# Optimization experiments

Measured on AMD Instinct MI355X. Metric: run time of the kernel, lower is better.

Reference implementation:

```python
import jax, jax.numpy as jnp
import numpy as np

# ---- static config (from init_kwargs) ----
XB = (-51.2, 51.2, 0.8); YB = (-51.2, 51.2, 0.8); ZB = (-10.0, 10.0, 20.0); DB = (1.0, 60.0, 1.0)
OGH, OGW = 256, 704          # image_size
DS = 16                      # downsample
C_IN, C_TR = 512, 64         # numC_input, numC_trans
B, N = 2, 6                  # batch, cameras
FH, FW = (OGH + DS - 1) // DS, (OGW + DS - 1) // DS   # 16, 44
DBINS = int(np.arange(DB[0], DB[1], DB[2]).shape[0])  # 59 depth bins
NX = int(round((XB[1] - XB[0]) / XB[2]))              # 128
NY = int(round((YB[1] - YB[0]) / YB[2]))              # 128
NZ = int(round((ZB[1] - ZB[0]) / ZB[2]))              # 1
START = jnp.array([XB[0], YB[0], ZB[0]], jnp.float32)
INTERVAL = jnp.array([XB[2], YB[2], ZB[2]], jnp.float32)

def make_frustum():
    ds = np.arange(DB[0], DB[1], DB[2], dtype=np.float32)            # [D]
    xs = np.linspace(0.0, OGW - 1, FW, dtype=np.float32)             # [FW]
    ys = np.linspace(0.0, OGH - 1, FH, dtype=np.float32)             # [FH]
    x, y, d = np.broadcast_arrays(xs[None, None, :], ys[None, :, None], ds[:, None, None])
    return jnp.asarray(np.stack([x, y, d], -1))                      # [D,FH,FW,3]

FRUSTUM = make_frustum()


def setup_inputs() -> dict:
    key = jax.random.key(0)
    k1, k2, k3 = jax.random.split(key, 3)
    x = jax.random.normal(k1, (B, N, C_IN, FH, FW), jnp.float32)
    # camera->ego rotation: cam z -> ego x, cam x -> -ego y, cam y -> -ego z
    R = jnp.array([[0., 0., 1.], [-1., 0., 0.], [0., -1., 0.]], jnp.float32)
    rots = jnp.broadcast_to(R, (B, N, 3, 3))
    trans = 0.5 * jax.random.normal(k2, (B, N, 3), jnp.float32)
    K = jnp.array([[500., 0., OGW / 2.], [0., 500., OGH / 2.], [0., 0., 1.]], jnp.float32)
    intrins = jnp.broadcast_to(K, (B, N, 3, 3))
    fan = C_IN + DBINS + C_TR
    w_depth = jax.random.normal(k3, (DBINS + C_TR, C_IN), jnp.float32) * np.float32(np.sqrt(2.0 / fan))
    b_depth = jnp.zeros((DBINS + C_TR,), jnp.float32)
    return {"x": x, "rots": rots, "trans": trans, "intrins": intrins,
            "w_depth": w_depth, "b_depth": b_depth}


def reference(x, rots, trans, intrins, w_depth, b_depth):
    # ---- geometry: frustum pixel coords -> ego frame (get_geometry) ----
    pts = jnp.concatenate([FRUSTUM[..., :2] * FRUSTUM[..., 2:3], FRUSTUM[..., 2:3]], -1)  # [D,FH,FW,3]
    combine = rots @ jnp.linalg.inv(intrins)                                              # [B,N,3,3]
    geom = jnp.einsum('bnij,dhwj->bndhwi', combine, pts) + trans[:, :, None, None, None, :]
    # ---- depth-weighted feature volume (get_volume) ----
    xf = x.reshape(B * N, C_IN, FH, FW)
    feat = jnp.einsum('oc,bchw->bohw', w_depth, xf) + b_depth[None, :, None, None]        # 1x1 conv
    depth = jax.nn.softmax(feat[:, :DBINS], axis=1)                                       # [BN,D,H,W]
    ctx = feat[:, DBINS:DBINS + C_TR]                                                     # [BN,C,H,W]
    vol = depth[:, None] * ctx[:, :, None]                                                # [BN,C,D,H,W]
    vol = vol.reshape(B, N, C_TR, DBINS, FH, FW).transpose(0, 1, 3, 4, 5, 2)              # [B,N,D,H,W,C]
    # ---- voxel pooling: sort/cumsum trick == per-voxel segment-sum scatter ----
    g = jnp.trunc((geom - START) / INTERVAL).astype(jnp.int32).reshape(-1, 3)             # trunc == torch .long()
    P = g.shape[0]
    b_ix = jnp.repeat(jnp.arange(B, dtype=jnp.int32), P // B)
    kept = ((g[:, 0] >= 0) & (g[:, 0] < NX) & (g[:, 1] >= 0) & (g[:, 1] < NY)
            & (g[:, 2] >= 0) & (g[:, 2] < NZ))
    total = B * NZ * NX * NY
    flat = ((b_ix * NZ + g[:, 2]) * NX + g[:, 0]) * NY + g[:, 1]                          # bev[b,gz,gx,gy]
    flat = jnp.where(kept, flat, total)                                                   # invalid -> dummy slot
    feats = jnp.where(kept[:, None], vol.reshape(-1, C_TR), 0.0)
    bev = jnp.zeros((total + 1, C_TR), vol.dtype).at[flat].add(feats)[:total]
    bev = bev.reshape(B, NZ, NX, NY, C_TR).transpose(0, 4, 1, 2, 3)                       # [B,C,NZ,NX,NY]
    return bev.reshape(B, C_TR * NZ, NX, NY)
```

## Files before the change

### kernel.cpp

```cpp
#include <hip/hip_runtime.h>
#include <cstddef>
#include <cstdint>
#include <math.h>

#define C_IN   512
#define C_TR   64
#define DBINS  59
#define NO     123
#define NOP    128
#define FH     16
#define FW     44
#define NPIX   704
#define NCAM   6
#define NBATCH 2
#define NBN    12
#define NXG    128
#define NYG    128
#define NCH    4
#define KCH    (C_IN/NCH)

#define WS_CMB     0
#define WS_XS      128
#define WS_YS      176

#define WSP_PART   256
#define PART_SZ    (NCH*NBN*NPIX*NOP)
#define WSP_DEP    (WSP_PART + PART_SZ)
#define DEP_SZ     (NBN*NPIX*C_TR)
#define WSP_CTX    (WSP_DEP + DEP_SZ)
#define WSP_BEV    (WSP_CTX + DEP_SZ)
#define BEV_SZ     (NBATCH*NXG*NYG*C_TR)
#define WS_FAST_TOTALF (WSP_BEV + BEV_SZ)

#define WS_FEAT    256
#define WS_CTX     (WS_FEAT + NBN*NOP*NPIX)
#define WS_BEV     (WS_CTX + NBN*NPIX*C_TR)

__global__ __launch_bounds__(256) void zero_kernel(float4* __restrict__ p, int n4)
{
  int i = blockIdx.x * 256 + threadIdx.x;
  const int stride = gridDim.x * 256;
  for (; i < n4; i += stride) p[i] = make_float4(0.f, 0.f, 0.f, 0.f);
}

__global__ __launch_bounds__(64) void prep_kernel(
    const float* __restrict__ rots, const float* __restrict__ intrins,
    float* __restrict__ wsf)
{
#pragma clang fp contract(off)
  int t = threadIdx.x;
  if (t < NBN) {
    const float* K = intrins + t * 9;
    const float* R = rots + t * 9;
    float A[3][3] = {{K[0],K[1],K[2]},{K[3],K[4],K[5]},{K[6],K[7],K[8]}};
    int piv[3] = {0,1,2};
    for (int k = 0; k < 2; ++k) {
      int p = k; float mx = fabsf(A[k][k]);
      for (int r = k+1; r < 3; ++r) { float v = fabsf(A[r][k]); if (v > mx) { mx = v; p = r; } }
      if (p != k) {
        for (int j = 0; j < 3; ++j) { float tmp = A[k][j]; A[k][j] = A[p][j]; A[p][j] = tmp; }
        int ti = piv[k]; piv[k] = piv[p]; piv[p] = ti;
      }
      float rk = 1.0f / A[k][k];
      for (int r = k+1; r < 3; ++r) {
        float l = A[r][k] * rk;
        A[r][k] = l;
        for (int j = k+1; j < 3; ++j) A[r][j] = A[r][j] - l * A[k][j];
      }
    }
    float r0 = 1.0f / A[0][0], r1 = 1.0f / A[1][1], r2 = 1.0f / A[2][2];
    float inv[3][3];
    for (int j = 0; j < 3; ++j) {
      float b0 = (piv[0]==j) ? 1.0f : 0.0f;
      float b1 = (piv[1]==j) ? 1.0f : 0.0f;
      float b2 = (piv[2]==j) ? 1.0f : 0.0f;
      float y0 = b0;
      float y1 = b1 - A[1][0]*y0;
      float y2 = (b2 - A[2][0]*y0) - A[2][1]*y1;
      float x2 = y2 * r2;
      float x1 = (y1 - A[1][2]*x2) * r1;
      float x0 = ((y0 - A[0][1]*x1) - A[0][2]*x2) * r0;
      inv[0][j] = x0; inv[1][j] = x1; inv[2][j] = x2;
    }
    float* cm = wsf + WS_CMB + t * 9;
    #pragma unroll
    for (int i = 0; i < 3; ++i)
      #pragma unroll
      for (int j = 0; j < 3; ++j)
        cm[i*3+j] = (R[i*3+0]*inv[0][j] + R[i*3+1]*inv[1][j]) + R[i*3+2]*inv[2][j];
  }
  if (t < FW) wsf[WS_XS + t] = (t == FW-1) ? 703.0f : (float)((double)t * (703.0 / 43.0));
  if (t < FH) wsf[WS_YS + t] = (t == FH-1) ? 255.0f : (float)((double)t * 17.0);
}

__global__ __launch_bounds__(256) void gemm_split_kernel(
    const float* __restrict__ x, const float* __restrict__ w,
    float* __restrict__ partial)
{
  __shared__ float smem[1024 + 32*132];
  float (*Xs)[32]   = (float(*)[32])smem;
  float (*WsT)[132] = (float(*)[132])(smem + 1024);
  const int bn  = blockIdx.y;
  const int ch  = blockIdx.z;
  const int hw0 = blockIdx.x * 32;
  const int t   = threadIdx.x;
  const int tx  = t & 7;
  const int ty  = t >> 3;
  float acc[4][4] = {};
  const float* xb = x + (size_t)bn * C_IN * NPIX;
  const int k0c = ch * KCH;

  for (int ks = 0; ks < KCH; ks += 32) {
    const int k0 = k0c + ks;
    #pragma unroll
    for (int i = 0; i < 4; ++i) {
      int k = (t >> 5) + i * 8;
      Xs[k][t & 31] = xb[(size_t)(k0 + k) * NPIX + hw0 + (t & 31)];
    }
    #pragma unroll
    for (int i = 0; i < 16; ++i) {
      int o = (t >> 5) + i * 8;
      WsT[t & 31][o] = (o < NO) ? w[(size_t)o * C_IN + k0 + (t & 31)] : 0.0f;
    }
    __syncthreads();
    #pragma unroll
    for (int k = 0; k < 32; ++k) {
      float4 xa = *(const float4*)&Xs[k][tx*4];
      float4 wv = *(const float4*)&WsT[k][ty*4];
      acc[0][0] += wv.x*xa.x; acc[0][1] += wv.x*xa.y; acc[0][2] += wv.x*xa.z; acc[0][3] += wv.x*xa.w;
      acc[1][0] += wv.y*xa.x; acc[1][1] += wv.y*xa.y; acc[1][2] += wv.y*xa.z; acc[1][3] += wv.y*xa.w;
      acc[2][0] += wv.z*xa.x; acc[2][1] += wv.z*xa.y; acc[2][2] += wv.z*xa.z; acc[2][3] += wv.z*xa.w;
      acc[3][0] += wv.w*xa.x; acc[3][1] += wv.w*xa.y; acc[3][2] += wv.w*xa.z; acc[3][3] += wv.w*xa.w;
    }
    __syncthreads();
  }
  float (*PT)[128] = (float(*)[128])smem;
  #pragma unroll
  for (int j = 0; j < 4; ++j) {
    float4 v = make_float4(acc[0][j], acc[1][j], acc[2][j], acc[3][j]);
    *(float4*)&PT[tx*4 + j][ty*4] = v;
  }
  __syncthreads();
  float* dst = partial + ((size_t)(ch*NBN + bn) * NPIX + hw0) * NOP;
  #pragma unroll
  for (int p = 0; p < 4; ++p) {
    int pix = (t >> 5) + p * 8;
    int o4  = (t & 31) * 4;
    *(float4*)&dst[(size_t)pix * NOP + o4] = *(const float4*)&PT[pix][o4];
  }
}

__global__ __launch_bounds__(256) void combine_kernel(
    const float* __restrict__ partial, const float* __restrict__ bias,
    float* __restrict__ depth, float* __restrict__ ctx_t)
{
  const int gid  = (int)((blockIdx.x * blockDim.x + threadIdx.x) >> 6);
  const int lane = threadIdx.x & 63;
  if (gid >= NBN * NPIX) return;
  const int bn  = gid / NPIX;
  const int pix = gid - bn * NPIX;

  float v0 = 0.0f, v1 = 0.0f;
  #pragma unroll
  for (int ch = 0; ch < NCH; ++ch) {
    const float* p = partial + ((size_t)(ch*NBN + bn) * NPIX + pix) * NOP;
    v0 += p[lane];
    v1 += p[lane + 64];
  }
  v0 += bias[lane];
  v1 += (lane + 64 < NO) ? bias[lane + 64] : 0.0f;

  float logit = (lane < DBINS) ? v0 : -__builtin_inff();
  float m = logit;
  #pragma unroll
  for (int off = 32; off; off >>= 1) m = fmaxf(m, __shfl_xor(m, off, 64));
  float e = (lane < DBINS) ? expf(logit - m) : 0.0f;
  float s = e;
  #pragma unroll
  for (int off = 32; off; off >>= 1) s += __shfl_xor(s, off, 64);

  if (lane < DBINS) depth[(size_t)gid * C_TR + lane] = e / s;

  float a  = __shfl(v0, (DBINS + lane) & 63, 64);
  float b2 = __shfl(v1, (DBINS + lane - 64) & 63, 64);
  float ctxv = (lane < 5) ? a : b2;
  ctx_t[(size_t)gid * C_TR + lane] = ctxv;
}

__global__ __launch_bounds__(256) void agg_kernel(
    const float* __restrict__ wsf, const float* __restrict__ trans,
    const float* __restrict__ dep, const float* __restrict__ ctx,
    float* __restrict__ bev, size_t sBN, size_t sD, size_t sP)
{
#pragma clang fp contract(off)
  const int wid = (int)((blockIdx.x * blockDim.x + threadIdx.x) >> 6);
  const int lane = threadIdx.x & 63;
  if (wid >= NBN * FW * DBINS) return;
  const int bn  = wid / (FW * DBINS);
  const int rem = wid - bn * (FW * DBINS);
  const int col = rem / DBINS;
  const int dm1 = rem - col * DBINS;
  const int b   = bn / NCAM;

  const float* cm = wsf + WS_CMB + bn * 9;
  const float* tr = trans + bn * 3;
  const float dd = 1.0f + (float)dm1;
  const float px = wsf[WS_XS + col] * dd;
  const float py0 = wsf[WS_YS + 0] * dd;
  const float e0 = (cm[0]*px + cm[1]*py0) + cm[2]*dd;
  const float e1 = (cm[3]*px + cm[4]*py0) + cm[5]*dd;
  const float g0 = e0 + tr[0];
  const float g1 = e1 + tr[1];
  const int gx = (int)truncf((g0 + 51.2f) / 0.8f);
  const int gy = (int)truncf((g1 + 51.2f) / 0.8f);
  if (gx < 0 || gx >= NXG || gy < 0 || gy >= NYG) return;

  const int r = lane & 15;
  const float pyr = wsf[WS_YS + r] * dd;
  const float e2 = (cm[6]*px + cm[7]*pyr) + cm[8]*dd;
  const float g2 = e2 + tr[2];
  const int gz = (int)truncf((g2 + 10.0f) / 20.0f);
  unsigned long long mask = __ballot(gz == 0) & 0xFFFFull;
  if (mask == 0) return;

  const float dep_r = dep[(size_t)bn * sBN + (size_t)dm1 * sD + (size_t)(r*FW + col) * sP];
  const float* ctxbase = ctx + ((size_t)bn * NPIX + col) * C_TR + lane;

  float acc = 0.0f;
  #pragma unroll
  for (int row = 0; row < FH; ++row) {
    if ((mask >> row) & 1ull) {
      float dv = __shfl(dep_r, row, 64);
      acc += dv * ctxbase[(size_t)(row * FW) * C_TR];
    }
  }
  atomicAdd(&bev[(((size_t)(b*NXG + gx) * NYG + gy) * C_TR) + lane], acc);
}

__global__ __launch_bounds__(256) void transpose_kernel(
    const float* __restrict__ bev, float* __restrict__ out)
{
  __shared__ float tile[NYG][C_TR + 1];
  const int b  = blockIdx.x >> 7;
  const int gx = blockIdx.x & 127;
  const float* src = bev + ((size_t)(b * NXG + gx) * NYG) * C_TR;
  const int t = threadIdx.x;
  #pragma unroll
  for (int i = 0; i < 32; ++i) {
    int idx = t + i * 256;
    tile[idx >> 6][idx & 63] = src[idx];
  }
  __syncthreads();
  const int lane = t & 63;
  const int cw   = t >> 6;
  size_t obase = (size_t)b * (C_TR*NXG*NYG) + (size_t)gx * NYG;
  #pragma unroll
  for (int i = 0; i < 16; ++i) {
    int c = cw + i * 4;
    out[obase + (size_t)c * (NXG*NYG) + lane]      = tile[lane][c];
    out[obase + (size_t)c * (NXG*NYG) + 64 + lane] = tile[64 + lane][c];
  }
}

__global__ __launch_bounds__(256) void gemm_fb_kernel(
    const float* __restrict__ x, const float* __restrict__ w,
    const float* __restrict__ bias, float* __restrict__ feat,
    float* __restrict__ ctx_t)
{
  __shared__ float Xs[64][32];
  __shared__ float Ws[128][66];
  __shared__ float CtxT[32][C_TR];
  const int bn  = blockIdx.y;
  const int hw0 = blockIdx.x * 32;
  const int t   = threadIdx.x;
  const int tx  = t & 7;
  const int ty  = t >> 3;
  float acc[4][4] = {};
  const float* xb = x + (size_t)bn * C_IN * NPIX;

  for (int k0 = 0; k0 < C_IN; k0 += 64) {
    #pragma unroll
    for (int i = 0; i < 8; ++i) {
      int r = (t >> 5) + i * 8;
      Xs[r][t & 31] = xb[(size_t)(k0 + r) * NPIX + hw0 + (t & 31)];
    }
    #pragma unroll
    for (int i = 0; i < 32; ++i) {
      int o = (t >> 6) + i * 4;
      Ws[o][t & 63] = (o < NO) ? w[(size_t)o * C_IN + k0 + (t & 63)] : 0.0f;
    }
    __syncthreads();
    #pragma unroll 8
    for (int k = 0; k < 64; k += 2) {
      float4 xa = *(const float4*)&Xs[k][tx*4];
      float4 xc = *(const float4*)&Xs[k+1][tx*4];
      #pragma unroll
      for (int i = 0; i < 4; ++i) {
        float2 wv = *(const float2*)&Ws[ty*4+i][k];
        acc[i][0] += wv.x*xa.x; acc[i][1] += wv.x*xa.y;
        acc[i][2] += wv.x*xa.z; acc[i][3] += wv.x*xa.w;
        acc[i][0] += wv.y*xc.x; acc[i][1] += wv.y*xc.y;
        acc[i][2] += wv.y*xc.z; acc[i][3] += wv.y*xc.w;
      }
    }
    __syncthreads();
  }
  #pragma unroll
  for (int i = 0; i < 4; ++i) {
    int o = ty*4 + i;
    float bb = (o < NO) ? bias[o] : 0.0f;
    float4 v = make_float4(acc[i][0]+bb, acc[i][1]+bb, acc[i][2]+bb, acc[i][3]+bb);
    *(float4*)&feat[((size_t)bn * NOP + o) * NPIX + hw0 + tx*4] = v;
    if (o >= DBINS && o < NO) {
      int c = o - DBINS;
      CtxT[tx*4+0][c] = v.x; CtxT[tx*4+1][c] = v.y;
      CtxT[tx*4+2][c] = v.z; CtxT[tx*4+3][c] = v.w;
    }
  }
  __syncthreads();
  const float* src = &CtxT[0][0];
  float* dst = ctx_t + ((size_t)bn * NPIX + hw0) * C_TR;
  #pragma unroll
  for (int k = 0; k < 2; ++k) {
    int f = (t + 256*k) * 4;
    *(float4*)&dst[f] = *(const float4*)&src[f];
  }
}

__global__ __launch_bounds__(256) void softmax_fb_kernel(float* __restrict__ feat)
{
  const int gwid = (int)((blockIdx.x * blockDim.x + threadIdx.x) >> 6);
  const int lane = threadIdx.x & 63;
  if (gwid >= NBN * NPIX) return;
  const int bn = gwid / NPIX;
  const int hw = gwid - bn * NPIX;
  float* fb = feat + (size_t)bn * NOP * NPIX + hw;
  float logit = (lane < DBINS) ? fb[(size_t)lane * NPIX] : -__builtin_inff();
  float m = logit;
  #pragma unroll
  for (int off = 32; off; off >>= 1) m = fmaxf(m, __shfl_xor(m, off, 64));
  float e = (lane < DBINS) ? expf(logit - m) : 0.0f;
  float s = e;
  #pragma unroll
  for (int off = 32; off; off >>= 1) s += __shfl_xor(s, off, 64);
  if (lane < DBINS) fb[(size_t)lane * NPIX] = e / s;
}

extern "C" void kernel_launch(void* const* d_in, const int* in_sizes, int n_in,
                              void* d_out, int out_size, void* d_ws, size_t ws_size,
                              hipStream_t stream)
{
  const float* x       = (const float*)d_in[0];
  const float* rots    = (const float*)d_in[1];
  const float* trans   = (const float*)d_in[2];
  const float* intrins = (const float*)d_in[3];
  const float* wd      = (const float*)d_in[4];
  const float* bd      = (const float*)d_in[5];
  float* out = (float*)d_out;
  float* wsf = (float*)d_ws;

  prep_kernel<<<1, 64, 0, stream>>>(rots, intrins, wsf);

  if (ws_size >= (size_t)WS_FAST_TOTALF * sizeof(float)) {
    float* part  = wsf + WSP_PART;
    float* depth = wsf + WSP_DEP;
    float* ctx_t = wsf + WSP_CTX;
    float* bev   = wsf + WSP_BEV;
    zero_kernel<<<2048, 256, 0, stream>>>((float4*)bev, BEV_SZ/4);
    gemm_split_kernel<<<dim3(NPIX/32, NBN, NCH), 256, 0, stream>>>(x, wd, part);
    combine_kernel<<<(NBN*NPIX)/4, 256, 0, stream>>>(part, bd, depth, ctx_t);
    agg_kernel<<<(NBN*FW*DBINS + 3)/4, 256, 0, stream>>>(
        wsf, trans, depth, ctx_t, bev,
        (size_t)NPIX * C_TR, (size_t)1, (size_t)C_TR);
    transpose_kernel<<<NBATCH*NXG, 256, 0, stream>>>(bev, out);
  } else {
    float* feat  = wsf + WS_FEAT;
    float* ctx_t = wsf + WS_CTX;
    float* bev   = wsf + WS_BEV;
    zero_kernel<<<2048, 256, 0, stream>>>((float4*)bev, BEV_SZ/4);
    gemm_fb_kernel<<<dim3(NPIX/32, NBN), 256, 0, stream>>>(x, wd, bd, feat, ctx_t);
    softmax_fb_kernel<<<(NBN*NPIX)/4, 256, 0, stream>>>(feat);
    agg_kernel<<<(NBN*FW*DBINS + 3)/4, 256, 0, stream>>>(
        wsf, trans, feat, ctx_t, bev,
        (size_t)NOP * NPIX, (size_t)NPIX, (size_t)1);
    transpose_kernel<<<NBATCH*NXG, 256, 0, stream>>>(bev, out);
  }
}
```

Baseline: 79.65 us.

## Retile split-K GEMM to 8x8 per thread, double K splits, fold prep into zero kernel

The split-K projection GEMM now gives each thread an 8x8 register tile over a 64-pixel block with 128 threads, instead of a 4x4 tile over 32 pixels. Outputs are written straight from registers without the shared-memory transpose. The K dimension is split into 8 chunks instead of 4, which keeps the block count the same. The camera prep work is merged into the BEV zeroing kernel to remove one launch. The cost is that the partial-sum buffer doubles, so the combine kernel reads twice as much data. The direct stores are less coalesced, and the larger workspace requirement may push execution onto the fallback path.

```diff
diff --git a/kernel.cpp b/kernel.cpp
--- a/kernel.cpp
+++ b/kernel.cpp
@@ -16,7 +16,7 @@
 #define NBN    12
 #define NXG    128
 #define NYG    128
-#define NCH    4
+#define NCH    8
 #define KCH    (C_IN/NCH)
 
 #define WS_CMB     0
@@ -36,19 +36,11 @@
 #define WS_CTX     (WS_FEAT + NBN*NOP*NPIX)
 #define WS_BEV     (WS_CTX + NBN*NPIX*C_TR)
 
-__global__ __launch_bounds__(256) void zero_kernel(float4* __restrict__ p, int n4)
-{
-  int i = blockIdx.x * 256 + threadIdx.x;
-  const int stride = gridDim.x * 256;
-  for (; i < n4; i += stride) p[i] = make_float4(0.f, 0.f, 0.f, 0.f);
-}
-
-__global__ __launch_bounds__(64) void prep_kernel(
-    const float* __restrict__ rots, const float* __restrict__ intrins,
-    float* __restrict__ wsf)
+__device__ void prep_body(const float* __restrict__ rots,
+                          const float* __restrict__ intrins,
+                          float* __restrict__ wsf, int t)
 {
 #pragma clang fp contract(off)
-  int t = threadIdx.x;
   if (t < NBN) {
     const float* K = intrins + t * 9;
     const float* R = rots + t * 9;
@@ -93,60 +85,71 @@
   if (t < FH) wsf[WS_YS + t] = (t == FH-1) ? 255.0f : (float)((double)t * 17.0);
 }
 
-__global__ __launch_bounds__(256) void gemm_split_kernel(
+__global__ __launch_bounds__(256) void zero_prep_kernel(
+    float4* __restrict__ bevp, int n4,
+    const float* __restrict__ rots, const float* __restrict__ intrins,
+    float* __restrict__ wsf)
+{
+  int i = blockIdx.x * 256 + threadIdx.x;
+  const int stride = gridDim.x * 256;
+  for (; i < n4; i += stride) bevp[i] = make_float4(0.f, 0.f, 0.f, 0.f);
+  if (blockIdx.x == 0 && threadIdx.x < 64)
+    prep_body(rots, intrins, wsf, threadIdx.x);
+}
+
+__global__ __launch_bounds__(128) void gemm_split_kernel(
     const float* __restrict__ x, const float* __restrict__ w,
     float* __restrict__ partial)
 {
-  __shared__ float smem[1024 + 32*132];
-  float (*Xs)[32]   = (float(*)[32])smem;
-  float (*WsT)[132] = (float(*)[132])(smem + 1024);
+  __shared__ float Xs[32][64];
+  __shared__ float WsT[32][132];
   const int bn  = blockIdx.y;
   const int ch  = blockIdx.z;
-  const int hw0 = blockIdx.x * 32;
+  const int hw0 = blockIdx.x * 64;
   const int t   = threadIdx.x;
-  const int tx  = t & 7;
-  const int ty  = t >> 3;
-  float acc[4][4] = {};
+  const int px0 = (t & 7) * 8;
+  const int oy0 = (t >> 3) * 8;
+  float acc[8][8] = {};
   const float* xb = x + (size_t)bn * C_IN * NPIX;
   const int k0c = ch * KCH;
 
   for (int ks = 0; ks < KCH; ks += 32) {
     const int k0 = k0c + ks;
     #pragma unroll
-    for (int i = 0; i < 4; ++i) {
-      int k = (t >> 5) + i * 8;
-      Xs[k][t & 31] = xb[(size_t)(k0 + k) * NPIX + hw0 + (t & 31)];
-    }
-    #pragma unroll
     for (int i = 0; i < 16; ++i) {
-      int o = (t >> 5) + i * 8;
-      WsT[t & 31][o] = (o < NO) ? w[(size_t)o * C_IN + k0 + (t & 31)] : 0.0f;
+      int idx = t + i * 128;
+      Xs[idx >> 6][idx & 63] = xb[(size_t)(k0 + (idx >> 6)) * NPIX + hw0 + (idx & 63)];
+    }
+    #pragma unroll
+    for (int i = 0; i < 32; ++i) {
+      int idx = t + i * 128;
+      int o = idx >> 5, k = idx & 31;
+      WsT[k][o] = (o < NO) ? w[(size_t)o * C_IN + k0 + k] : 0.0f;
     }
     __syncthreads();
     #pragma unroll
     for (int k = 0; k < 32; ++k) {
-      float4 xa = *(const float4*)&Xs[k][tx*4];
-      float4 wv = *(const float4*)&WsT[k][ty*4];
-      acc[0][0] += wv.x*xa.x; acc[0][1] += wv.x*xa.y; acc[0][2] += wv.x*xa.z; acc[0][3] += wv.x*xa.w;
-      acc[1][0] += wv.y*xa.x; acc[1][1] += wv.y*xa.y; acc[1][2] += wv.y*xa.z; acc[1][3] += wv.y*xa.w;
-      acc[2][0] += wv.z*xa.x; acc[2][1] += wv.z*xa.y; acc[2][2] += wv.z*xa.z; acc[2][3] += wv.z*xa.w;
-      acc[3][0] += wv.w*xa.x; acc[3][1] += wv.w*xa.y; acc[3][2] += wv.w*xa.z; acc[3][3] += wv.w*xa.w;
+      float4 xa = *(const float4*)&Xs[k][px0];
+      float4 xc = *(const float4*)&Xs[k][px0 + 4];
+      float4 wa = *(const float4*)&WsT[k][oy0];
+      float4 wb = *(const float4*)&WsT[k][oy0 + 4];
+      float xv[8] = {xa.x,xa.y,xa.z,xa.w,xc.x,xc.y,xc.z,xc.w};
+      float wv[8] = {wa.x,wa.y,wa.z,wa.w,wb.x,wb.y,wb.z,wb.w};
+      #pragma unroll
+      for (int i = 0; i < 8; ++i)
+        #pragma unroll
+        for (int j = 0; j < 8; ++j)
+          acc[i][j] += wv[i] * xv[j];
     }
     __syncthreads();
   }
-  float (*PT)[128] = (float(*)[128])smem;
-  #pragma unroll
-  for (int j = 0; j < 4; ++j) {
-    float4 v = make_float4(acc[0][j], acc[1][j], acc[2][j], acc[3][j]);
-    *(float4*)&PT[tx*4 + j][ty*4] = v;
-  }
-  __syncthreads();
   float* dst = partial + ((size_t)(ch*NBN + bn) * NPIX + hw0) * NOP;
   #pragma unroll
-  for (int p = 0; p < 4; ++p) {
-    int pix = (t >> 5) + p * 8;
-    int o4  = (t & 31) * 4;
-    *(float4*)&dst[(size_t)pix * NOP + o4] = *(const float4*)&PT[pix][o4];
+  for (int j = 0; j < 8; ++j) {
+    float4 v0 = make_float4(acc[0][j], acc[1][j], acc[2][j], acc[3][j]);
+    float4 v1 = make_float4(acc[4][j], acc[5][j], acc[6][j], acc[7][j]);
+    *(float4*)&dst[(size_t)(px0 + j) * NOP + oy0]     = v0;
+    *(float4*)&dst[(size_t)(px0 + j) * NOP + oy0 + 4] = v1;
   }
 }
 
@@ -359,15 +362,13 @@
   float* out = (float*)d_out;
   float* wsf = (float*)d_ws;
 
-  prep_kernel<<<1, 64, 0, stream>>>(rots, intrins, wsf);
-
   if (ws_size >= (size_t)WS_FAST_TOTALF * sizeof(float)) {
     float* part  = wsf + WSP_PART;
     float* depth = wsf + WSP_DEP;
     float* ctx_t = wsf + WSP_CTX;
     float* bev   = wsf + WSP_BEV;
-    zero_kernel<<<2048, 256, 0, stream>>>((float4*)bev, BEV_SZ/4);
-    gemm_split_kernel<<<dim3(NPIX/32, NBN, NCH), 256, 0, stream>>>(x, wd, part);
+    zero_prep_kernel<<<2048, 256, 0, stream>>>((float4*)bev, BEV_SZ/4, rots, intrins, wsf);
+    gemm_split_kernel<<<dim3(NPIX/64, NBN, NCH), 128, 0, stream>>>(x, wd, part);
     combine_kernel<<<(NBN*NPIX)/4, 256, 0, stream>>>(part, bd, depth, ctx_t);
     agg_kernel<<<(NBN*FW*DBINS + 3)/4, 256, 0, stream>>>(
         wsf, trans, depth, ctx_t, bev,
@@ -377,7 +378,7 @@
     float* feat  = wsf + WS_FEAT;
     float* ctx_t = wsf + WS_CTX;
     float* bev   = wsf + WS_BEV;
-    zero_kernel<<<2048, 256, 0, stream>>>((float4*)bev, BEV_SZ/4);
+    zero_prep_kernel<<<2048, 256, 0, stream>>>((float4*)bev, BEV_SZ/4, rots, intrins, wsf);
     gemm_fb_kernel<<<dim3(NPIX/32, NBN), 256, 0, stream>>>(x, wd, bd, feat, ctx_t);
     softmax_fb_kernel<<<(NBN*NPIX)/4, 256, 0, stream>>>(feat);
     agg_kernel<<<(NBN*FW*DBINS + 3)/4, 256, 0, stream>>>(
```

Result: slower. 93.36 us (+17.2%).
